# Kernel optimization log

Measured on AMD Instinct MI355X. Metric: run time of the kernel, lower is better.

The kernel has to match this reference:

```python
import jax, jax.numpy as jnp
import numpy as np

N_NODES = 50000
N_EDGES = 1_600_000
IN_CH = 256
HEADS = 4
OUT_CH = 32


def setup_inputs() -> dict:
    key = jax.random.key(0)
    k1, k2, k3, k4 = jax.random.split(key, 4)
    x = jax.random.normal(k1, (N_NODES, IN_CH), dtype=jnp.float32)
    edge_index = jax.random.randint(k2, (2, N_EDGES), 0, N_NODES, dtype=jnp.int32)
    # xavier-uniform-like init scales
    W = jax.random.uniform(k3, (IN_CH, HEADS * OUT_CH), dtype=jnp.float32,
                           minval=-1.0, maxval=1.0) * np.sqrt(6.0 / (IN_CH + HEADS * OUT_CH))
    attn = jax.random.uniform(k4, (HEADS, 2 * OUT_CH), dtype=jnp.float32,
                              minval=-1.0, maxval=1.0) * np.sqrt(6.0 / (HEADS + 2 * OUT_CH))
    return {"x": x, "edge_index": edge_index, "W": W, "attn": attn}


def reference(x, edge_index, W, attn):
    n = x.shape[0]
    H = attn.shape[0]
    C = attn.shape[1] // 2
    # h = lin(x).view(n, H, C)
    h = (x @ W).reshape(n, H, C)
    row, col = edge_index[0], edge_index[1]
    # (cat([h_row, h_col]) * attn).sum(-1) == h_row.a_src + h_col.a_dst;
    # compute per-node scores then gather per edge (cheaper, same math).
    a_src, a_dst = attn[:, :C], attn[:, C:]
    s_src = jnp.einsum('nhc,hc->nh', h, a_src)  # [n, H]
    s_dst = jnp.einsum('nhc,hc->nh', h, a_dst)  # [n, H]
    alpha = jax.nn.leaky_relu(s_src[row] + s_dst[col], 0.2)  # [E, H]
    # segment softmax over edges grouped by target node `row`
    seg_max = jax.ops.segment_max(alpha, row, num_segments=n)  # [n, H]
    ex = jnp.exp(alpha - seg_max[row])
    denom = jax.ops.segment_sum(ex, row, num_segments=n)  # [n, H]
    alpha_norm = ex / denom[row]  # [E, H]
    # weighted scatter-add of source features (dropout p=0.0 is identity)
    out = jax.ops.segment_sum(alpha_norm[..., None] * h[col], row, num_segments=n)  # [n,H,C]
    return out.mean(axis=1), alpha_norm
```

## Files before the change

### kernel.cpp

```cpp
#include <hip/hip_runtime.h>

#define NNODES 50000
#define NEDGES 1600000
#define IN_CH 256
#define HEADS 4
#define OUT_CH 32
#define HC 128
#define NSB ((NNODES + 255) / 256)
#define NCHUNK 128
#define CE 12500
#define WORDS 25000

typedef unsigned int u32;
typedef unsigned short u16;
typedef short bf16x8 __attribute__((ext_vector_type(8)));
typedef u16 u16x8 __attribute__((ext_vector_type(8)));
typedef float f32x4 __attribute__((ext_vector_type(4)));

__device__ __forceinline__ float b2f(u16 s) { return __uint_as_float(((u32)s) << 16); }
__device__ __forceinline__ u16 f2b(float f) {
  u32 u = __float_as_uint(f);
  u32 r = (u + 0x7FFFu + ((u >> 16) & 1u)) >> 16;
  return (u16)r;
}
__device__ __forceinline__ float lrelu(float v) { return v >= 0.f ? v : 0.2f * v; }

#define NR 16

__global__ __launch_bounds__(256) void k_wprep(const float* __restrict__ W,
                                               u16* __restrict__ wt) {
  int i = blockIdx.x * 256 + threadIdx.x;
  if (i >= IN_CH * HC) return;
  int kk = i & 31;
  int n = (i >> 5) & 127;
  int kt = i >> 12;
  wt[i] = f2b(W[(size_t)(kt * 32 + kk) * HC + n]);
}

__global__ __launch_bounds__(256) void k_gemm(const float* __restrict__ x,
                                              const u16* __restrict__ wt,
                                              const float* __restrict__ attn,
                                              u16* __restrict__ hb,
                                              float* __restrict__ nrec) {
  __shared__ union {
    struct {
      u16 xh[64 * 32];
      u16 xl[64 * 32];
      u16 wh[128 * 32];
    } st;
    float cbuf[64 * 132];
  } L;
  __shared__ float sA[256];
  const int tid = threadIdx.x;
  const int wave = tid >> 6;
  const int lane = tid & 63;
  const int row0 = blockIdx.x * 64;
  sA[tid] = attn[tid];

  f32x4 acc[4][2] = {};
  const int frow = lane & 15;
  const int koff = (lane >> 4) << 4;

  const int sr = tid >> 2;
  const int skc = (tid & 3) << 3;
  const int sgrow = row0 + sr;
  const int sxb = (sr << 6) + (skc << 1);
  const int sxs = sxb ^ ((sr & 7) << 4);

  for (int kt = 0; kt < 8; ++kt) {
    {
      float4 v0 = make_float4(0.f, 0.f, 0.f, 0.f), v1 = v0;
      if (sgrow < NNODES) {
        const float* px = &x[(size_t)sgrow * IN_CH + kt * 32 + skc];
        v0 = *(const float4*)px;
        v1 = *(const float4*)(px + 4);
      }
      float vv[8] = {v0.x, v0.y, v0.z, v0.w, v1.x, v1.y, v1.z, v1.w};
      u16x8 hi, lo;
#pragma unroll
      for (int i = 0; i < 8; ++i) {
        u16 h = f2b(vv[i]);
        hi[i] = h;
        lo[i] = f2b(vv[i] - b2f(h));
      }
      *(u16x8*)((char*)L.st.xh + sxs) = hi;
      *(u16x8*)((char*)L.st.xl + sxs) = lo;
    }
#pragma unroll
    for (int li = 0; li < 2; ++li) {
      int i = tid + (li << 8);
      int col = i >> 2;
      int kb = (i & 3) << 4;
      u16x8 v = *(const u16x8*)((const char*)wt + (((size_t)(kt * 128 + col)) << 6) + kb);
      int sb = ((col << 6) + kb) ^ ((col & 7) << 4);
      *(u16x8*)((char*)L.st.wh + sb) = v;
    }
    __syncthreads();
    bf16x8 ah[4], al[4], bw[2];
#pragma unroll
    for (int mi = 0; mi < 4; ++mi) {
      int r = mi * 16 + frow;
      int sb = ((r << 6) + koff) ^ ((r & 7) << 4);
      ah[mi] = *(bf16x8*)((char*)L.st.xh + sb);
      al[mi] = *(bf16x8*)((char*)L.st.xl + sb);
    }
#pragma unroll
    for (int ni = 0; ni < 2; ++ni) {
      int c = (wave << 5) + ni * 16 + frow;
      int sb = ((c << 6) + koff) ^ ((c & 7) << 4);
      bw[ni] = *(bf16x8*)((char*)L.st.wh + sb);
    }
#pragma unroll
    for (int mi = 0; mi < 4; ++mi)
#pragma unroll
      for (int ni = 0; ni < 2; ++ni) {
        acc[mi][ni] = __builtin_amdgcn_mfma_f32_16x16x32_bf16(ah[mi], bw[ni], acc[mi][ni], 0, 0, 0);
        acc[mi][ni] = __builtin_amdgcn_mfma_f32_16x16x32_bf16(al[mi], bw[ni], acc[mi][ni], 0, 0, 0);
      }
    __syncthreads();
  }

#pragma unroll
  for (int mi = 0; mi < 4; ++mi)
#pragma unroll
    for (int ni = 0; ni < 2; ++ni) {
#pragma unroll
      for (int reg = 0; reg < 4; ++reg) {
        int row = mi * 16 + ((lane >> 4) << 2) + reg;
        int col = (wave << 5) + (ni << 4) + frow;
        L.cbuf[row * 132 + col] = acc[mi][ni][reg];
      }
    }
  __syncthreads();

  const int tc = tid & 31;
  const int tr = tid >> 5;
  const int head = tc >> 3;
  const int cb = (tc & 7) << 2;
  const float4 as4 = *(const float4*)&sA[head * 64 + cb];
  const float4 ad4 = *(const float4*)&sA[head * 64 + 32 + cb];
#pragma unroll
  for (int i = 0; i < 8; ++i) {
    int row = (tr << 3) + i;
    int grow = row0 + row;
    float4 v = *(const float4*)&L.cbuf[row * 132 + (tc << 2)];
    float ps = v.x * as4.x + v.y * as4.y + v.z * as4.z + v.w * as4.w;
    float pd = v.x * ad4.x + v.y * ad4.y + v.z * ad4.z + v.w * ad4.w;
    ps += __shfl_xor(ps, 1); ps += __shfl_xor(ps, 2); ps += __shfl_xor(ps, 4);
    pd += __shfl_xor(pd, 1); pd += __shfl_xor(pd, 2); pd += __shfl_xor(pd, 4);
    if (grow < NNODES) {
      u16 q[4] = {f2b(v.x), f2b(v.y), f2b(v.z), f2b(v.w)};
      *(ushort4*)&hb[(size_t)grow * HC + (tc << 2)] = *(ushort4*)q;
      if ((tc & 7) == 0) {
        nrec[(size_t)grow * NR + head] = ps;
        nrec[(size_t)grow * NR + 4 + head] = pd;
      }
    }
  }
}

__global__ __launch_bounds__(256) void k_chist(const int* __restrict__ rowi,
                                               u32* __restrict__ chunk_hist,
                                               u16* __restrict__ lslot) {
  __shared__ u32 lh[WORDS];
  const int c = blockIdx.x;
  const int tid = threadIdx.x;
  for (int i = tid; i < WORDS; i += 256) lh[i] = 0;
  __syncthreads();
  const int base = c * CE;
  for (int i = tid; i < CE; i += 256) {
    int e = base + i;
    int r = rowi[e];
    u32 sh = (u32)(r & 1) << 4;
    u32 old = atomicAdd(&lh[r >> 1], 1u << sh);
    lslot[e] = (u16)((old >> sh) & 0xFFFFu);
  }
  __syncthreads();
  u32* dst = chunk_hist + (size_t)c * WORDS;
  for (int i = tid; i < WORDS; i += 256) dst[i] = lh[i];
}

__global__ __launch_bounds__(256) void k_cscan(u32* __restrict__ chunk_hist,
                                               int* __restrict__ counts) {
  __shared__ u32 tile[NCHUNK][64];
  const int w0 = blockIdx.x * 64;
  const int tid = threadIdx.x;
  for (int i = tid; i < NCHUNK * 64; i += 256) {
    int c = i >> 6, wl = i & 63;
    int w = w0 + wl;
    tile[c][wl] = (w < WORDS) ? chunk_hist[(size_t)c * WORDS + w] : 0u;
  }
  __syncthreads();
  if (tid < 64) {
    u32 slo = 0, shi = 0;
    for (int c = 0; c < NCHUNK; ++c) {
      u32 v = tile[c][tid];
      tile[c][tid] = slo | (shi << 16);
      slo += v & 0xFFFFu;
      shi += v >> 16;
    }
    int w = w0 + tid;
    if (w < WORDS) {
      int r = w << 1;
      if (r < NNODES) counts[r] = (int)slo;
      if (r + 1 < NNODES) counts[r + 1] = (int)shi;
    }
  }
  __syncthreads();
  for (int i = tid; i < NCHUNK * 64; i += 256) {
    int c = i >> 6, wl = i & 63;
    int w = w0 + wl;
    if (w < WORDS) chunk_hist[(size_t)c * WORDS + w] = tile[c][wl];
  }
}

__global__ __launch_bounds__(256) void k_scan1(const int* __restrict__ counts,
                                               int* __restrict__ bsum) {
  int i = blockIdx.x * 256 + threadIdx.x;
  int v = (i < NNODES) ? counts[i] : 0;
#pragma unroll
  for (int m = 1; m < 64; m <<= 1) v += __shfl_xor(v, m);
  __shared__ int ws[4];
  if ((threadIdx.x & 63) == 0) ws[threadIdx.x >> 6] = v;
  __syncthreads();
  if (threadIdx.x == 0) bsum[blockIdx.x] = ws[0] + ws[1] + ws[2] + ws[3];
}

__global__ __launch_bounds__(256) void k_scan2(const int* __restrict__ bsum,
                                               int* __restrict__ boff) {
  __shared__ int s[256];
  int t = threadIdx.x;
  int v = (t < NSB) ? bsum[t] : 0;
  s[t] = v;
  __syncthreads();
  for (int off = 1; off < 256; off <<= 1) {
    int u = (t >= off) ? s[t - off] : 0;
    __syncthreads();
    s[t] += u;
    __syncthreads();
  }
  boff[t] = s[t] - v;
}

__global__ __launch_bounds__(256) void k_scan3(const int* __restrict__ counts,
                                               const int* __restrict__ boff,
                                               int* __restrict__ row_ptr) {
  __shared__ int s[256];
  int t = threadIdx.x;
  int i = blockIdx.x * 256 + t;
  int v = (i < NNODES) ? counts[i] : 0;
  s[t] = v;
  __syncthreads();
  for (int off = 1; off < 256; off <<= 1) {
    int u = (t >= off) ? s[t - off] : 0;
    __syncthreads();
    s[t] += u;
    __syncthreads();
  }
  if (i < NNODES) row_ptr[i] = boff[blockIdx.x] + s[t] - v;
  if (i == 0) row_ptr[NNODES] = NEDGES;
}

__global__ void k_scatter(const int* __restrict__ rowi, const int* __restrict__ coli,
                          const int* __restrict__ row_ptr,
                          const u32* __restrict__ chunk_hist,
                          const u16* __restrict__ lslot,
                          u16* __restrict__ col_csr) {
  int e = blockIdx.x * 256 + threadIdx.x;
  if (e >= NEDGES) return;
  int r = rowi[e];
  int c = e / CE;
  u32 word = chunk_hist[(size_t)c * WORDS + (r >> 1)];
  int off = (int)((word >> ((u32)(r & 1) << 4)) & 0xFFFFu);
  int pos = row_ptr[r] + off + (int)lslot[e];
  col_csr[pos] = (u16)coli[e];
}

__global__ __launch_bounds__(256) void k_softmax(const u16* __restrict__ col_csr,
                                                 const int* __restrict__ row_ptr,
                                                 float* __restrict__ nrec,
                                                 u16* __restrict__ an16) {
  const int wid = threadIdx.x >> 6;
  const int lane = threadIdx.x & 63;
  const int r = blockIdx.x * 4 + wid;
  if (r >= NNODES) return;
  const int p0 = row_ptr[r], p1 = row_ptr[r + 1];
  const int deg = p1 - p0;
  if (deg == 0) return;
  const float4 ss = *(const float4*)&nrec[(size_t)r * NR];
  const float NEG = -3.0e38f;

  if (deg <= 64) {
    float4 al = make_float4(NEG, NEG, NEG, NEG);
    if (lane < deg) {
      int c = col_csr[p0 + lane];
      float4 sd = *(const float4*)&nrec[(size_t)c * NR + 4];
      al.x = lrelu(ss.x + sd.x);
      al.y = lrelu(ss.y + sd.y);
      al.z = lrelu(ss.z + sd.z);
      al.w = lrelu(ss.w + sd.w);
    }
    float4 mx = al;
#pragma unroll
    for (int m = 1; m < 64; m <<= 1) {
      mx.x = fmaxf(mx.x, __shfl_xor(mx.x, m));
      mx.y = fmaxf(mx.y, __shfl_xor(mx.y, m));
      mx.z = fmaxf(mx.z, __shfl_xor(mx.z, m));
      mx.w = fmaxf(mx.w, __shfl_xor(mx.w, m));
    }
    float4 ex = make_float4(0.f, 0.f, 0.f, 0.f);
    if (lane < deg) {
      ex.x = __expf(al.x - mx.x);
      ex.y = __expf(al.y - mx.y);
      ex.z = __expf(al.z - mx.z);
      ex.w = __expf(al.w - mx.w);
    }
    float4 sm = ex;
#pragma unroll
    for (int m = 1; m < 64; m <<= 1) {
      sm.x += __shfl_xor(sm.x, m);
      sm.y += __shfl_xor(sm.y, m);
      sm.z += __shfl_xor(sm.z, m);
      sm.w += __shfl_xor(sm.w, m);
    }
    float4 rd = make_float4(1.f / sm.x, 1.f / sm.y, 1.f / sm.z, 1.f / sm.w);
    if (lane == 0) {
      *(float4*)&nrec[(size_t)r * NR + 8] = mx;
      *(float4*)&nrec[(size_t)r * NR + 12] = rd;
    }
    if (lane < deg) {
      u16 q[4] = {f2b(ex.x * rd.x), f2b(ex.y * rd.y), f2b(ex.z * rd.z), f2b(ex.w * rd.w)};
      *(ushort4*)&an16[(size_t)(p0 + lane) * 4] = *(ushort4*)q;
    }
  } else {
    float4 mx = make_float4(NEG, NEG, NEG, NEG);
    for (int p = p0 + lane; p < p1; p += 64) {
      int c = col_csr[p];
      float4 sd = *(const float4*)&nrec[(size_t)c * NR + 4];
      mx.x = fmaxf(mx.x, lrelu(ss.x + sd.x));
      mx.y = fmaxf(mx.y, lrelu(ss.y + sd.y));
      mx.z = fmaxf(mx.z, lrelu(ss.z + sd.z));
      mx.w = fmaxf(mx.w, lrelu(ss.w + sd.w));
    }
#pragma unroll
    for (int m = 1; m < 64; m <<= 1) {
      mx.x = fmaxf(mx.x, __shfl_xor(mx.x, m));
      mx.y = fmaxf(mx.y, __shfl_xor(mx.y, m));
      mx.z = fmaxf(mx.z, __shfl_xor(mx.z, m));
      mx.w = fmaxf(mx.w, __shfl_xor(mx.w, m));
    }
    float4 sm = make_float4(0.f, 0.f, 0.f, 0.f);
    for (int p = p0 + lane; p < p1; p += 64) {
      int c = col_csr[p];
      float4 sd = *(const float4*)&nrec[(size_t)c * NR + 4];
      sm.x += __expf(lrelu(ss.x + sd.x) - mx.x);
      sm.y += __expf(lrelu(ss.y + sd.y) - mx.y);
      sm.z += __expf(lrelu(ss.z + sd.z) - mx.z);
      sm.w += __expf(lrelu(ss.w + sd.w) - mx.w);
    }
#pragma unroll
    for (int m = 1; m < 64; m <<= 1) {
      sm.x += __shfl_xor(sm.x, m);
      sm.y += __shfl_xor(sm.y, m);
      sm.z += __shfl_xor(sm.z, m);
      sm.w += __shfl_xor(sm.w, m);
    }
    float4 rd = make_float4(1.f / sm.x, 1.f / sm.y, 1.f / sm.z, 1.f / sm.w);
    if (lane == 0) {
      *(float4*)&nrec[(size_t)r * NR + 8] = mx;
      *(float4*)&nrec[(size_t)r * NR + 12] = rd;
    }
    for (int p = p0 + lane; p < p1; p += 64) {
      int c = col_csr[p];
      float4 sd = *(const float4*)&nrec[(size_t)c * NR + 4];
      float4 ex;
      ex.x = __expf(lrelu(ss.x + sd.x) - mx.x) * rd.x;
      ex.y = __expf(lrelu(ss.y + sd.y) - mx.y) * rd.y;
      ex.z = __expf(lrelu(ss.z + sd.z) - mx.z) * rd.z;
      ex.w = __expf(lrelu(ss.w + sd.w) - mx.w) * rd.w;
      u16 q[4] = {f2b(ex.x), f2b(ex.y), f2b(ex.z), f2b(ex.w)};
      *(ushort4*)&an16[(size_t)p * 4] = *(ushort4*)q;
    }
  }
}

__global__ void k_alphaf(const int* __restrict__ rowi, const int* __restrict__ coli,
                         const float* __restrict__ nrec,
                         float* __restrict__ alpha_out) {
  int e = blockIdx.x * 256 + threadIdx.x;
  if (e >= NEDGES) return;
  int r = rowi[e], c = coli[e];
  const float* nr = &nrec[(size_t)r * NR];
  float4 ss = *(const float4*)(nr);
  float4 m4 = *(const float4*)(nr + 8);
  float4 rd = *(const float4*)(nr + 12);
  float4 sd = *(const float4*)&nrec[(size_t)c * NR + 4];
  float4 an;
  an.x = __expf(lrelu(ss.x + sd.x) - m4.x) * rd.x;
  an.y = __expf(lrelu(ss.y + sd.y) - m4.y) * rd.y;
  an.z = __expf(lrelu(ss.z + sd.z) - m4.z) * rd.z;
  an.w = __expf(lrelu(ss.w + sd.w) - m4.w) * rd.w;
  *(float4*)&alpha_out[(size_t)e * 4] = an;
}

__global__ __launch_bounds__(256) void k_aggr(const u16* __restrict__ col_csr,
                                              const int* __restrict__ row_ptr,
                                              const u16* __restrict__ an16,
                                              const u16* __restrict__ hb,
                                              float* __restrict__ out_mean) {
  const int wid = threadIdx.x >> 6;
  const int lane = threadIdx.x & 63;
  const int r = blockIdx.x * 4 + wid;
  if (r >= NNODES) return;
  const int p0 = row_ptr[r], p1 = row_ptr[r + 1];
  const int hd = lane >> 4;
  const int ch = lane << 1;
  float acc0 = 0.f, acc1 = 0.f;

  int p = p0;
  for (; p + 8 <= p1; p += 8) {
    int cs[8];
    float ws[8];
    u32 hv[8];
#pragma unroll
    for (int i = 0; i < 8; ++i) cs[i] = col_csr[p + i];
#pragma unroll
    for (int i = 0; i < 8; ++i) ws[i] = b2f(an16[(size_t)(p + i) * 4 + hd]);
#pragma unroll
    for (int i = 0; i < 8; ++i) hv[i] = *(const u32*)&hb[(size_t)cs[i] * HC + ch];
#pragma unroll
    for (int i = 0; i < 8; ++i) {
      acc0 += ws[i] * b2f((u16)(hv[i] & 0xFFFFu));
      acc1 += ws[i] * b2f((u16)(hv[i] >> 16));
    }
  }
  for (; p < p1; ++p) {
    int c = col_csr[p];
    float w = b2f(an16[(size_t)p * 4 + hd]);
    u32 hv = *(const u32*)&hb[(size_t)c * HC + ch];
    acc0 += w * b2f((u16)(hv & 0xFFFFu));
    acc1 += w * b2f((u16)(hv >> 16));
  }
  acc0 += __shfl_xor(acc0, 16);
  acc0 += __shfl_xor(acc0, 32);
  acc1 += __shfl_xor(acc1, 16);
  acc1 += __shfl_xor(acc1, 32);
  if (lane < 16) {
    float2 o = make_float2(acc0 * 0.25f, acc1 * 0.25f);
    *(float2*)&out_mean[(size_t)r * 32 + (lane << 1)] = o;
  }
}

extern "C" void kernel_launch(void* const* d_in, const int* in_sizes, int n_in,
                              void* d_out, int out_size, void* d_ws, size_t ws_size,
                              hipStream_t stream) {
  const float* x = (const float*)d_in[0];
  const int* ei = (const int*)d_in[1];
  const float* W = (const float*)d_in[2];
  const float* attn = (const float*)d_in[3];
  const int* rowi = ei;
  const int* coli = ei + NEDGES;

  float* out_mean = (float*)d_out;
  float* alpha_out = (float*)d_out + (size_t)NNODES * 32;

  char* w = (char*)d_ws;
  u16* hb = (u16*)w;          w += (size_t)NNODES * HC * 2;
  u16* an16 = (u16*)w;        w += (size_t)NEDGES * 4 * 2;
  float* nrec = (float*)w;    w += (size_t)NNODES * NR * 4;
  int* counts = (int*)w;      w += (size_t)NNODES * 4;
  int* bsum = (int*)w;        w += (size_t)256 * 4;
  int* boff = (int*)w;        w += (size_t)256 * 4;
  int* row_ptr = (int*)w;     w += (size_t)50016 * 4;
  u16* lslot = (u16*)w;       w += (size_t)NEDGES * 2;
  u16* col_csr = (u16*)w;     w += (size_t)NEDGES * 2;
  u32* chunk_hist = (u32*)w;  w += (size_t)NCHUNK * WORDS * 4;
  u16* wt = (u16*)w;          w += (size_t)IN_CH * HC * 2;

  k_wprep<<<(IN_CH * HC + 255) / 256, 256, 0, stream>>>(W, wt);
  k_gemm<<<(NNODES + 63) / 64, 256, 0, stream>>>(x, wt, attn, hb, nrec);
  k_chist<<<NCHUNK, 256, 0, stream>>>(rowi, chunk_hist, lslot);
  k_cscan<<<(WORDS + 63) / 64, 256, 0, stream>>>(chunk_hist, counts);
  k_scan1<<<NSB, 256, 0, stream>>>(counts, bsum);
  k_scan2<<<1, 256, 0, stream>>>(bsum, boff);
  k_scan3<<<NSB, 256, 0, stream>>>(counts, boff, row_ptr);
  k_scatter<<<(NEDGES + 255) / 256, 256, 0, stream>>>(rowi, coli, row_ptr, chunk_hist, lslot, col_csr);
  k_softmax<<<(NNODES + 3) / 4, 256, 0, stream>>>(col_csr, row_ptr, nrec, an16);
  k_alphaf<<<(NEDGES + 255) / 256, 256, 0, stream>>>(rowi, coli, nrec, alpha_out);
  k_aggr<<<(NNODES + 3) / 4, 256, 0, stream>>>(col_csr, row_ptr, an16, hb, out_mean);
}
```

Baseline: 225.5 us.

## Merge independent kernels into shared launches via block-range dispatch

The GEMM and the CSR scatter, which do not depend on each other, now run in one launch: blocks past the GEMM range perform the scatter, each handling four edges per thread. Likewise, the per-edge alpha output computation and the CSR aggregation now share one launch. The GEMM is moved after the scan kernels so that both halves of the merged launch have their inputs ready. The intent is to remove launch gaps and let memory-bound scatter/alpha blocks overlap with compute-bound or latency-bound blocks, at the cost of higher LDS and register allocation for the lightweight blocks, which could reduce their occupancy.

```diff
diff --git a/kernel.cpp b/kernel.cpp
--- a/kernel.cpp
+++ b/kernel.cpp
@@ -11,6 +11,11 @@
 #define CE 12500
 #define WORDS 25000
 
+#define GEMM_BLOCKS ((NNODES + 63) / 64)
+#define SCAT_BLOCKS ((NEDGES + 1023) / 1024)
+#define AGGR_BLOCKS ((NNODES + 3) / 4)
+#define ALPHA_BLOCKS ((NEDGES + 255) / 256)
+
 typedef unsigned int u32;
 typedef unsigned short u16;
 typedef short bf16x8 __attribute__((ext_vector_type(8)));
@@ -37,11 +42,17 @@
   wt[i] = f2b(W[(size_t)(kt * 32 + kk) * HC + n]);
 }
 
-__global__ __launch_bounds__(256) void k_gemm(const float* __restrict__ x,
-                                              const u16* __restrict__ wt,
-                                              const float* __restrict__ attn,
-                                              u16* __restrict__ hb,
-                                              float* __restrict__ nrec) {
+__global__ __launch_bounds__(256) void k_gemscat(const float* __restrict__ x,
+                                                 const u16* __restrict__ wt,
+                                                 const float* __restrict__ attn,
+                                                 u16* __restrict__ hb,
+                                                 float* __restrict__ nrec,
+                                                 const int* __restrict__ rowi,
+                                                 const int* __restrict__ coli,
+                                                 const int* __restrict__ row_ptr,
+                                                 const u32* __restrict__ chunk_hist,
+                                                 const u16* __restrict__ lslot,
+                                                 u16* __restrict__ col_csr) {
   __shared__ union {
     struct {
       u16 xh[64 * 32];
@@ -52,6 +63,24 @@
   } L;
   __shared__ float sA[256];
   const int tid = threadIdx.x;
+
+  if (blockIdx.x >= GEMM_BLOCKS) {
+    const int base = (blockIdx.x - GEMM_BLOCKS) * 1024 + tid;
+#pragma unroll
+    for (int k = 0; k < 4; ++k) {
+      int e = base + k * 256;
+      if (e < NEDGES) {
+        int r = rowi[e];
+        int c = e / CE;
+        u32 word = chunk_hist[(size_t)c * WORDS + (r >> 1)];
+        int off = (int)((word >> ((u32)(r & 1) << 4)) & 0xFFFFu);
+        int pos = row_ptr[r] + off + (int)lslot[e];
+        col_csr[pos] = (u16)coli[e];
+      }
+    }
+    return;
+  }
+
   const int wave = tid >> 6;
   const int lane = tid & 63;
   const int row0 = blockIdx.x * 64;
@@ -261,21 +290,6 @@
   if (i == 0) row_ptr[NNODES] = NEDGES;
 }
 
-__global__ void k_scatter(const int* __restrict__ rowi, const int* __restrict__ coli,
-                          const int* __restrict__ row_ptr,
-                          const u32* __restrict__ chunk_hist,
-                          const u16* __restrict__ lslot,
-                          u16* __restrict__ col_csr) {
-  int e = blockIdx.x * 256 + threadIdx.x;
-  if (e >= NEDGES) return;
-  int r = rowi[e];
-  int c = e / CE;
-  u32 word = chunk_hist[(size_t)c * WORDS + (r >> 1)];
-  int off = (int)((word >> ((u32)(r & 1) << 4)) & 0xFFFFu);
-  int pos = row_ptr[r] + off + (int)lslot[e];
-  col_csr[pos] = (u16)coli[e];
-}
-
 __global__ __launch_bounds__(256) void k_softmax(const u16* __restrict__ col_csr,
                                                  const int* __restrict__ row_ptr,
                                                  float* __restrict__ nrec,
@@ -384,30 +398,32 @@
   }
 }
 
-__global__ void k_alphaf(const int* __restrict__ rowi, const int* __restrict__ coli,
-                         const float* __restrict__ nrec,
-                         float* __restrict__ alpha_out) {
-  int e = blockIdx.x * 256 + threadIdx.x;
-  if (e >= NEDGES) return;
-  int r = rowi[e], c = coli[e];
-  const float* nr = &nrec[(size_t)r * NR];
-  float4 ss = *(const float4*)(nr);
-  float4 m4 = *(const float4*)(nr + 8);
-  float4 rd = *(const float4*)(nr + 12);
-  float4 sd = *(const float4*)&nrec[(size_t)c * NR + 4];
-  float4 an;
-  an.x = __expf(lrelu(ss.x + sd.x) - m4.x) * rd.x;
-  an.y = __expf(lrelu(ss.y + sd.y) - m4.y) * rd.y;
-  an.z = __expf(lrelu(ss.z + sd.z) - m4.z) * rd.z;
-  an.w = __expf(lrelu(ss.w + sd.w) - m4.w) * rd.w;
-  *(float4*)&alpha_out[(size_t)e * 4] = an;
-}
-
-__global__ __launch_bounds__(256) void k_aggr(const u16* __restrict__ col_csr,
-                                              const int* __restrict__ row_ptr,
-                                              const u16* __restrict__ an16,
-                                              const u16* __restrict__ hb,
-                                              float* __restrict__ out_mean) {
+__global__ __launch_bounds__(256) void k_alphaggr(const u16* __restrict__ col_csr,
+                                                  const int* __restrict__ row_ptr,
+                                                  const u16* __restrict__ an16,
+                                                  const u16* __restrict__ hb,
+                                                  float* __restrict__ out_mean,
+                                                  const int* __restrict__ rowi,
+                                                  const int* __restrict__ coli,
+                                                  const float* __restrict__ nrec,
+                                                  float* __restrict__ alpha_out) {
+  if (blockIdx.x >= AGGR_BLOCKS) {
+    int e = (blockIdx.x - AGGR_BLOCKS) * 256 + threadIdx.x;
+    if (e >= NEDGES) return;
+    int r = rowi[e], c = coli[e];
+    const float* nr = &nrec[(size_t)r * NR];
+    float4 ss = *(const float4*)(nr);
+    float4 m4 = *(const float4*)(nr + 8);
+    float4 rd = *(const float4*)(nr + 12);
+    float4 sd = *(const float4*)&nrec[(size_t)c * NR + 4];
+    float4 an;
+    an.x = __expf(lrelu(ss.x + sd.x) - m4.x) * rd.x;
+    an.y = __expf(lrelu(ss.y + sd.y) - m4.y) * rd.y;
+    an.z = __expf(lrelu(ss.z + sd.z) - m4.z) * rd.z;
+    an.w = __expf(lrelu(ss.w + sd.w) - m4.w) * rd.w;
+    *(float4*)&alpha_out[(size_t)e * 4] = an;
+    return;
+  }
   const int wid = threadIdx.x >> 6;
   const int lane = threadIdx.x & 63;
   const int r = blockIdx.x * 4 + wid;
@@ -478,14 +494,14 @@
   u16* wt = (u16*)w;          w += (size_t)IN_CH * HC * 2;
 
   k_wprep<<<(IN_CH * HC + 255) / 256, 256, 0, stream>>>(W, wt);
-  k_gemm<<<(NNODES + 63) / 64, 256, 0, stream>>>(x, wt, attn, hb, nrec);
   k_chist<<<NCHUNK, 256, 0, stream>>>(rowi, chunk_hist, lslot);
   k_cscan<<<(WORDS + 63) / 64, 256, 0, stream>>>(chunk_hist, counts);
   k_scan1<<<NSB, 256, 0, stream>>>(counts, bsum);
   k_scan2<<<1, 256, 0, stream>>>(bsum, boff);
   k_scan3<<<NSB, 256, 0, stream>>>(counts, boff, row_ptr);
-  k_scatter<<<(NEDGES + 255) / 256, 256, 0, stream>>>(rowi, coli, row_ptr, chunk_hist, lslot, col_csr);
+  k_gemscat<<<GEMM_BLOCKS + SCAT_BLOCKS, 256, 0, stream>>>(
+      x, wt, attn, hb, nrec, rowi, coli, row_ptr, chunk_hist, lslot, col_csr);
   k_softmax<<<(NNODES + 3) / 4, 256, 0, stream>>>(col_csr, row_ptr, nrec, an16);
-  k_alphaf<<<(NEDGES + 255) / 256, 256, 0, stream>>>(rowi, coli, nrec, alpha_out);
-  k_aggr<<<(NNODES + 3) / 4, 256, 0, stream>>>(col_csr, row_ptr, an16, hb, out_mean);
-}
+  k_alphaggr<<<AGGR_BLOCKS + ALPHA_BLOCKS, 256, 0, stream>>>(
+      col_csr, row_ptr, an16, hb, out_mean, rowi, coli, nrec, alpha_out);
+}
```

After: 201.8 us. 1.12x faster.
